# Optimization experiments

Measured on AMD Instinct MI355X. Metric: run time of the kernel, lower is better.

The kernel has to match this reference:

```python
import jax, jax.numpy as jnp
import numpy as np

# Qwen3-Next style GatedDeltaNet config
H = 2048          # hidden_size
HV = 32           # num_v_heads
HK = 16           # num_k_heads
DK = 128          # head_k_dim
DV = 128          # head_v_dim
KW = 4            # conv kernel size
KEY_DIM = HK * DK
VAL_DIM = HV * DV
CONV_DIM = 2 * KEY_DIM + VAL_DIM
B, S = 2, 1024
EPS = 1e-6


def setup_inputs() -> dict:
    key = jax.random.key(0)
    ks = jax.random.split(key, 9)
    def rn(i, shape, scale):
        return jax.random.normal(ks[i], shape, jnp.float32) * scale
    return {
        "hidden_states": rn(0, (B, S, H), 1.0),
        "Wqkv": rn(1, (H, CONV_DIM), H ** -0.5),
        "Wz": rn(2, (H, VAL_DIM), H ** -0.5),
        "Wb": rn(3, (H, HV), H ** -0.5),
        "Wa": rn(4, (H, HV), H ** -0.5),
        "conv_w": rn(5, (CONV_DIM, KW), 0.3),
        "conv_b": jnp.zeros((CONV_DIM,), jnp.float32),
        "dt_bias": jnp.ones((HV,), jnp.float32),
        "A_log": jnp.log(jax.random.uniform(ks[6], (HV,), jnp.float32, 0.001, 16.0)),
        "norm_weight": jnp.ones((DV,), jnp.float32),
        "Wout": rn(7, (VAL_DIM, H), VAL_DIM ** -0.5),
    }


def _causal_depthwise_conv(x, w, b):
    # x: [B,S,C], w: [C,KW] depthwise, causal (left pad KW-1), then SiLU
    xp = jnp.pad(x, ((0, 0), (KW - 1, 0), (0, 0)))
    out = b
    for j in range(KW):
        out = out + xp[:, j:j + x.shape[1], :] * w[:, j]
    return jax.nn.silu(out)


def _l2norm(x):
    return x * jax.lax.rsqrt(jnp.sum(x * x, axis=-1, keepdims=True) + 1e-6)


def reference(hidden_states, Wqkv, Wz, Wb, Wa, conv_w, conv_b, dt_bias, A_log, norm_weight, Wout):
    x = hidden_states  # [B,S,H]
    mixed = _causal_depthwise_conv(x @ Wqkv, conv_w, conv_b)  # [B,S,CONV_DIM]
    q, k, v = jnp.split(mixed, [KEY_DIM, 2 * KEY_DIM], axis=-1)
    q = q.reshape(B, S, HK, DK)
    k = k.reshape(B, S, HK, DK)
    v = v.reshape(B, S, HV, DV)
    z = (x @ Wz).reshape(B, S, HV, DV)
    beta = jax.nn.sigmoid(x @ Wb)                                  # [B,S,HV]
    g = -jnp.exp(A_log) * jax.nn.softplus(x @ Wa + dt_bias)       # [B,S,HV]

    rep = HV // HK
    q = jnp.repeat(q, rep, axis=2)  # [B,S,HV,DK]
    k = jnp.repeat(k, rep, axis=2)
    q = _l2norm(q) * (DK ** -0.5)
    k = _l2norm(k)

    # gated delta-rule recurrence, state: [B,HV,DK,DV]
    def step(state, inp):
        qt, kt, vt, gt, bt = inp  # [B,HV,DK],[B,HV,DK],[B,HV,DV],[B,HV],[B,HV]
        state = state * jnp.exp(gt)[..., None, None]
        mem = jnp.einsum('bhk,bhkv->bhv', kt, state)
        delta = (vt - mem) * bt[..., None]
        state = state + jnp.einsum('bhk,bhv->bhkv', kt, delta)
        out_t = jnp.einsum('bhk,bhkv->bhv', qt, state)
        return state, out_t

    init = jnp.zeros((B, HV, DK, DV), jnp.float32)
    seq = (q.transpose(1, 0, 2, 3), k.transpose(1, 0, 2, 3), v.transpose(1, 0, 2, 3),
           g.transpose(1, 0, 2), beta.transpose(1, 0, 2))
    _, core = jax.lax.scan(step, init, seq)   # [S,B,HV,DV]
    core = core.transpose(1, 0, 2, 3)          # [B,S,HV,DV]

    # gated RMSNorm: gate with silu(z) then rms-normalize over head_v_dim
    gated = core * jax.nn.silu(z)
    var = jnp.mean(gated * gated, axis=-1, keepdims=True)
    normed = gated * jax.lax.rsqrt(var + EPS) * norm_weight

    return normed.reshape(B, S, VAL_DIM) @ Wout  # [B,S,H]
```

## Files before the change

### kernel.cpp

```cpp
#include <hip/hip_runtime.h>
#include <stdint.h>

typedef unsigned short u16;
typedef unsigned int u32;
typedef __attribute__((ext_vector_type(8))) short bf16x8;
typedef __attribute__((ext_vector_type(4))) float f32x4;

__device__ __forceinline__ float asf(u32 u) { union { u32 u; float f; } v; v.u = u; return v.f; }
__device__ __forceinline__ float bf2f(u16 h) { return asf(((u32)h) << 16); }
__device__ __forceinline__ u16 f2bf(float f) {
  union { float f; u32 u; } v; v.f = f;
  u32 r = v.u + 0x7fffu + ((v.u >> 16) & 1u);
  return (u16)(r >> 16);
}
__device__ __forceinline__ float silu(float x) { return x / (1.f + __expf(-x)); }

__device__ __forceinline__ void async16(void* lds, const void* g) {
  __builtin_amdgcn_global_load_lds(
      (__attribute__((address_space(1))) void*)g,
      (__attribute__((address_space(3))) void*)lds, 16, 0, 0);
}
__device__ __forceinline__ void async4(void* lds, const void* g) {
  __builtin_amdgcn_global_load_lds(
      (__attribute__((address_space(1))) void*)g,
      (__attribute__((address_space(3))) void*)lds, 4, 0, 0);
}

template <int CTRL>
__device__ __forceinline__ float dppadd(float x) {
  int y = __builtin_amdgcn_update_dpp(0, __float_as_int(x), CTRL, 0xf, 0xf, true);
  return x + __int_as_float(y);
}
__device__ __forceinline__ float redseg8(float x) {
  x = dppadd<0xB1>(x);
  x = dppadd<0x4E>(x);
  x = dppadd<0x141>(x);
  return x;
}
__device__ __forceinline__ float redseg16(float x) {
  x = dppadd<0xB1>(x);
  x = dppadd<0x4E>(x);
  x = dppadd<0x141>(x);
  x = dppadd<0x140>(x);
  return x;
}

__device__ __forceinline__ void unpack8(uint4 r, float* o) {
  o[0] = asf(r.x << 16); o[1] = asf(r.x & 0xffff0000u);
  o[2] = asf(r.y << 16); o[3] = asf(r.y & 0xffff0000u);
  o[4] = asf(r.z << 16); o[5] = asf(r.z & 0xffff0000u);
  o[6] = asf(r.w << 16); o[7] = asf(r.w & 0xffff0000u);
}

__global__ __launch_bounds__(256) void cvt_f32_bf16_k(
    const float* __restrict__ in, u16* __restrict__ out, int n8) {
  int i = blockIdx.x * 256 + threadIdx.x;
  if (i >= n8) return;
  const float4 a = *(const float4*)&in[(size_t)i * 8];
  const float4 b = *(const float4*)&in[(size_t)i * 8 + 4];
  u16 o[8] = {f2bf(a.x), f2bf(a.y), f2bf(a.z), f2bf(a.w),
              f2bf(b.x), f2bf(b.y), f2bf(b.z), f2bf(b.w)};
  *(uint4*)&out[(size_t)i * 8] = *(const uint4*)o;
}

__global__ __launch_bounds__(256) void transpose_cvt(
    const float* __restrict__ W, u16* __restrict__ WT, int R, int C) {
  __shared__ u16 tile[64][65];
  const int r0 = blockIdx.y * 64, c0 = blockIdx.x * 64;
  const int t = threadIdx.x;
  {
    const int lr = t >> 4;
    const int lc = (t & 15) * 4;
#pragma unroll
    for (int p = 0; p < 4; ++p) {
      int rr = lr + p * 16;
      float4 v = *(const float4*)&W[(size_t)(r0 + rr) * C + c0 + lc];
      tile[lc + 0][rr] = f2bf(v.x);
      tile[lc + 1][rr] = f2bf(v.y);
      tile[lc + 2][rr] = f2bf(v.z);
      tile[lc + 3][rr] = f2bf(v.w);
    }
  }
  __syncthreads();
  {
    const int wr = t >> 2;
    const int wc = (t & 3) * 16;
    u16 buf[16];
#pragma unroll
    for (int j = 0; j < 16; ++j) buf[j] = tile[wr][wc + j];
    u16* dst = &WT[(size_t)(c0 + wr) * R + r0 + wc];
    *(uint4*)(dst) = *(const uint4*)&buf[0];
    *(uint4*)(dst + 8) = *(const uint4*)&buf[8];
  }
}

template <int F32OUT>
__global__ __launch_bounds__(256) void gemm_mfma_bt(
    const u16* __restrict__ A, const u16* __restrict__ BT, void* __restrict__ Cout,
    int M, int N, int K) {
  __shared__ u16 As[128 * 32];
  __shared__ u16 Bs[128 * 32];
  const int tid = threadIdx.x;
  const int m0 = blockIdx.y * 128, n0 = blockIdx.x * 128;
  const int wave = tid >> 6, lane = tid & 63;
  const int wr = wave >> 1, wc = wave & 1;
  const int lrow = lane & 15, lgrp = lane >> 4;
  const int rsw = (lrow >> 1) & 3;

  f32x4 acc[4][4] = {};

  const int srow = tid >> 2;
  const int sslot = (tid & 3) ^ ((srow >> 1) & 3);
  const u16* gA0 = A + (size_t)(m0 + srow) * K + sslot * 8;
  const u16* gA1 = A + (size_t)(m0 + 64 + srow) * K + sslot * 8;
  const u16* gB0 = BT + (size_t)(n0 + srow) * K + sslot * 8;
  const u16* gB1 = BT + (size_t)(n0 + 64 + srow) * K + sslot * 8;
  u16* lA0 = As + tid * 8;
  u16* lA1 = As + 2048 + tid * 8;
  u16* lB0 = Bs + tid * 8;
  u16* lB1 = Bs + 2048 + tid * 8;

  int aoff[4], boff[4];
#pragma unroll
  for (int i = 0; i < 4; ++i) {
    int arow = wr * 64 + i * 16 + lrow;
    aoff[i] = arow * 64 + ((lgrp ^ rsw) << 4);
    int brow = wc * 64 + i * 16 + lrow;
    boff[i] = brow * 64 + ((lgrp ^ rsw) << 4);
  }

  for (int kt = 0; kt < K; kt += 32) {
    async16(lA0, gA0); async16(lA1, gA1);
    async16(lB0, gB0); async16(lB1, gB1);
    gA0 += 32; gA1 += 32; gB0 += 32; gB1 += 32;
    __syncthreads();
    bf16x8 af[4], bfr[4];
#pragma unroll
    for (int i = 0; i < 4; ++i) {
      af[i] = *(const bf16x8*)((const char*)As + aoff[i]);
      bfr[i] = *(const bf16x8*)((const char*)Bs + boff[i]);
    }
#pragma unroll
    for (int mi = 0; mi < 4; ++mi)
#pragma unroll
      for (int ni = 0; ni < 4; ++ni)
        acc[mi][ni] = __builtin_amdgcn_mfma_f32_16x16x32_bf16(af[mi], bfr[ni], acc[mi][ni], 0, 0, 0);
    __syncthreads();
  }

#pragma unroll
  for (int mi = 0; mi < 4; ++mi)
#pragma unroll
    for (int ni = 0; ni < 4; ++ni) {
      const int m = m0 + wr * 64 + mi * 16 + lgrp * 4;
      const int n = n0 + wc * 64 + ni * 16 + lrow;
      if (F32OUT) {
        float* C = (float*)Cout;
#pragma unroll
        for (int r = 0; r < 4; ++r)
          C[(size_t)(m + r) * N + n] = asf(((u32)f2bf(acc[mi][ni][r])) << 16);
      } else {
        u16* C = (u16*)Cout;
#pragma unroll
        for (int r = 0; r < 4; ++r)
          C[(size_t)(m + r) * N + n] = f2bf(acc[mi][ni][r]);
      }
    }
}

__global__ __launch_bounds__(256) void gemm_f32(
    const float* __restrict__ A, const float* __restrict__ B, u16* __restrict__ C,
    int M, int N, int K, int ldB) {
  __shared__ float As[32][68];
  __shared__ float Bs[32][68];
  const int tid = threadIdx.x;
  const int m0 = blockIdx.y * 64, n0 = blockIdx.x * 64;
  const int tx = tid & 15, ty = tid >> 4;
  float acc[4][4] = {};
  const int arow = tid >> 2, ac = (tid & 3) * 8;
  const int brow = tid >> 3, bc = (tid & 7) * 8;
  for (int kt = 0; kt < K; kt += 32) {
    const float* sa = &A[(size_t)(m0 + arow) * K + kt + ac];
    float4 a0 = *(const float4*)sa, a1 = *(const float4*)(sa + 4);
    As[ac + 0][arow] = a0.x; As[ac + 1][arow] = a0.y;
    As[ac + 2][arow] = a0.z; As[ac + 3][arow] = a0.w;
    As[ac + 4][arow] = a1.x; As[ac + 5][arow] = a1.y;
    As[ac + 6][arow] = a1.z; As[ac + 7][arow] = a1.w;
    const float* sb = &B[(size_t)(kt + brow) * ldB + n0 + bc];
    *(float4*)&Bs[brow][bc] = *(const float4*)sb;
    *(float4*)&Bs[brow][bc + 4] = *(const float4*)(sb + 4);
    __syncthreads();
#pragma unroll 8
    for (int kk = 0; kk < 32; ++kk) {
      float4 av = *(const float4*)&As[kk][ty * 4];
      float4 bv = *(const float4*)&Bs[kk][tx * 4];
      float a4[4] = {av.x, av.y, av.z, av.w};
      float b4[4] = {bv.x, bv.y, bv.z, bv.w};
#pragma unroll
      for (int i = 0; i < 4; ++i)
#pragma unroll
        for (int j = 0; j < 4; ++j) acc[i][j] += a4[i] * b4[j];
    }
    __syncthreads();
  }
#pragma unroll
  for (int i = 0; i < 4; ++i)
#pragma unroll
    for (int j = 0; j < 4; ++j)
      C[(size_t)(m0 + ty * 4 + i) * N + n0 + tx * 4 + j] = f2bf(acc[i][j]);
}

__global__ __launch_bounds__(256) void gemm_bf16A_f32(
    const u16* __restrict__ A, const float* __restrict__ B, float* __restrict__ C,
    int M, int N, int K, int ldB) {
  __shared__ float As[32][68];
  __shared__ float Bs[32][68];
  const int tid = threadIdx.x;
  const int m0 = blockIdx.y * 64, n0 = blockIdx.x * 64;
  const int tx = tid & 15, ty = tid >> 4;
  float acc[4][4] = {};
  const int arow = tid >> 2, ac = (tid & 3) * 8;
  const int brow = tid >> 3, bc = (tid & 7) * 8;
  for (int kt = 0; kt < K; kt += 32) {
    uint4 raw = *(const uint4*)&A[(size_t)(m0 + arow) * K + kt + ac];
    As[ac + 0][arow] = asf(raw.x << 16); As[ac + 1][arow] = asf(raw.x & 0xffff0000u);
    As[ac + 2][arow] = asf(raw.y << 16); As[ac + 3][arow] = asf(raw.y & 0xffff0000u);
    As[ac + 4][arow] = asf(raw.z << 16); As[ac + 5][arow] = asf(raw.z & 0xffff0000u);
    As[ac + 6][arow] = asf(raw.w << 16); As[ac + 7][arow] = asf(raw.w & 0xffff0000u);
    const float* sb = &B[(size_t)(kt + brow) * ldB + n0 + bc];
    *(float4*)&Bs[brow][bc] = *(const float4*)sb;
    *(float4*)&Bs[brow][bc + 4] = *(const float4*)(sb + 4);
    __syncthreads();
#pragma unroll 8
    for (int kk = 0; kk < 32; ++kk) {
      float4 av = *(const float4*)&As[kk][ty * 4];
      float4 bv = *(const float4*)&Bs[kk][tx * 4];
      float a4[4] = {av.x, av.y, av.z, av.w};
      float b4[4] = {bv.x, bv.y, bv.z, bv.w};
#pragma unroll
      for (int i = 0; i < 4; ++i)
#pragma unroll
        for (int j = 0; j < 4; ++j) acc[i][j] += a4[i] * b4[j];
    }
    __syncthreads();
  }
#pragma unroll
  for (int i = 0; i < 4; ++i)
#pragma unroll
    for (int j = 0; j < 4; ++j) {
      u32 r = (u32)f2bf(acc[i][j]) << 16;
      C[(size_t)(m0 + ty * 4 + i) * N + n0 + tx * 4 + j] = asf(r);
    }
}

__global__ __launch_bounds__(256) void betag_v2(
    const float* __restrict__ x, const float* __restrict__ Wb, const float* __restrict__ Wa,
    const float* __restrict__ dtb, const float* __restrict__ alog,
    float* __restrict__ beta, float* __restrict__ g) {
  __shared__ float part[256];
  const int token = blockIdx.x;
  const int t = threadIdx.x;
  const int o = t & 63;
  const int sl = t >> 6;
  const float* xrow = x + (size_t)token * 2048;
  const float* W = (o < 32) ? Wb : Wa;
  const int oc = o & 31;
  float acc = 0.f;
  const int k0 = sl * 512;
#pragma unroll 4
  for (int k = k0; k < k0 + 512; ++k) acc += xrow[k] * W[(size_t)k * 32 + oc];
  part[t] = acc;
  __syncthreads();
  if (t < 64) {
    float s = part[t] + part[t + 64] + part[t + 128] + part[t + 192];
    if (t < 32) {
      beta[(size_t)token * 32 + t] = 1.f / (1.f + __expf(-s));
    } else {
      int j = t - 32;
      float xx = s + dtb[j];
      float sp = (xx > 20.f) ? xx : log1pf(__expf(xx));
      g[(size_t)token * 32 + j] = -__expf(alog[j]) * sp;
    }
  }
}

__global__ __launch_bounds__(256) void conv_qk_v2(
    const u16* __restrict__ mixedQK, const float* __restrict__ cw, const float* __restrict__ cb,
    u16* __restrict__ qn, u16* __restrict__ kn) {
  __shared__ float qk[4096];
  const int token = blockIdx.x;
  const int s = token & 1023;
  const int t = threadIdx.x;
#pragma unroll
  for (int gi = 0; gi < 2; ++gi) {
    const int ch = t * 8 + gi * 2048;
    float acc[8];
    float w[8][4];
#pragma unroll
    for (int i = 0; i < 8; ++i) {
      acc[i] = cb[ch + i];
      float4 wv = *(const float4*)&cw[(size_t)(ch + i) * 4];
      w[i][0] = wv.x; w[i][1] = wv.y; w[i][2] = wv.z; w[i][3] = wv.w;
    }
#pragma unroll
    for (int j = 0; j < 4; ++j) {
      int sr = s - 3 + j;
      if (sr >= 0) {
        uint4 raw = *(const uint4*)&mixedQK[(size_t)(token - 3 + j) * 4096 + ch];
        float xv[8];
        unpack8(raw, xv);
#pragma unroll
        for (int i = 0; i < 8; ++i) acc[i] += w[i][j] * xv[i];
      }
    }
#pragma unroll
    for (int i = 0; i < 8; ++i) qk[ch + i] = silu(acc[i]);
  }
  __syncthreads();
  const int slot = t >> 3, m = t & 7;
  float vv[16];
#pragma unroll
  for (int i = 0; i < 16; i += 4) {
    float4 f = *(const float4*)&qk[slot * 128 + m * 16 + i];
    vv[i] = f.x; vv[i + 1] = f.y; vv[i + 2] = f.z; vv[i + 3] = f.w;
  }
  float ss = 0.f;
#pragma unroll
  for (int i = 0; i < 16; ++i) ss += vv[i] * vv[i];
  ss = redseg8(ss);
  float r = rsqrtf(ss + 1e-6f);
  u16 o[16];
  u16* dst;
  if (slot < 16) {
    r *= 0.08838834764831845f;
    dst = qn + (size_t)token * 2048 + slot * 128 + m * 16;
  } else {
    dst = kn + (size_t)token * 2048 + (slot - 16) * 128 + m * 16;
  }
#pragma unroll
  for (int i = 0; i < 16; ++i) o[i] = f2bf(vv[i] * r);
  *(uint4*)dst = *(const uint4*)&o[0];
  *(uint4*)(dst + 8) = *(const uint4*)&o[8];
}

__global__ __launch_bounds__(256) void conv_v_v2(
    const u16* __restrict__ mixedV, const float* __restrict__ cw, const float* __restrict__ cb,
    u16* __restrict__ vout) {
  const int token = blockIdx.x;
  const int s = token & 1023;
  const int t = threadIdx.x;
#pragma unroll
  for (int gi = 0; gi < 2; ++gi) {
    const int ch = t * 8 + gi * 2048;
    const int gch = 4096 + ch;
    float acc[8];
    float w[8][4];
#pragma unroll
    for (int i = 0; i < 8; ++i) {
      acc[i] = cb[gch + i];
      float4 wv = *(const float4*)&cw[(size_t)(gch + i) * 4];
      w[i][0] = wv.x; w[i][1] = wv.y; w[i][2] = wv.z; w[i][3] = wv.w;
    }
#pragma unroll
    for (int j = 0; j < 4; ++j) {
      int sr = s - 3 + j;
      if (sr >= 0) {
        uint4 raw = *(const uint4*)&mixedV[(size_t)(token - 3 + j) * 4096 + ch];
        float xv[8];
        unpack8(raw, xv);
#pragma unroll
        for (int i = 0; i < 8; ++i) acc[i] += w[i][j] * xv[i];
      }
    }
    u16 o[8];
#pragma unroll
    for (int i = 0; i < 8; ++i) o[i] = f2bf(silu(acc[i]));
    *(uint4*)&vout[(size_t)token * 4096 + ch] = *(const uint4*)o;
  }
}

#define SCAN_T 64
__global__ __launch_bounds__(512) void scan_lds2(
    const u16* __restrict__ qn, const u16* __restrict__ kn, const u16* __restrict__ v,
    const float* __restrict__ g, const float* __restrict__ beta,
    u16* __restrict__ core) {
  __shared__ u16 Kb[2][SCAN_T][128];
  __shared__ u16 Qb[2][SCAN_T][128];
  __shared__ u16 Vb[2][SCAN_T][32];
  __shared__ float Gb[2][SCAN_T];
  __shared__ float Bb[2][SCAN_T];

  const int blk = blockIdx.x;
  const int pair = blk >> 2, chunk = blk & 3;
  const int b = pair >> 5, h = pair & 31, kh = h >> 1;
  const int t = threadIdx.x;
  const int wave = t >> 6;
  const int lane = t & 63;
  const int seg = t & 15, dvl = t >> 4;
  const int dv = chunk * 32 + dvl;

  const size_t tok0 = (size_t)b * 1024;
  const u16* kbase = kn + tok0 * 2048 + (size_t)kh * 128;
  const u16* qbase = qn + tok0 * 2048 + (size_t)kh * 128;
  const u16* vbase = v + tok0 * 4096 + (size_t)h * 128 + chunk * 32;
  const float* gbase = g + tok0 * 32 + h;
  const float* bbase = beta + tok0 * 32 + h;
  u16* cp = core + tok0 * 4096 + (size_t)h * 128 + dv;

  auto stage = [&](int buf, int tile) {
    const int gt = tile * SCAN_T;
#pragma unroll
    for (int i = 0; i < 2; ++i) {
      int off = (i * 512 + t) * 16;
      int row = off >> 8;
      int c16 = (off >> 4) & 15;
      async16((char*)&Kb[buf][0][0] + off,
              (const char*)(kbase + (size_t)(gt + row) * 2048) + c16 * 16);
      async16((char*)&Qb[buf][0][0] + off,
              (const char*)(qbase + (size_t)(gt + row) * 2048) + c16 * 16);
    }
    if (t < 256) {
      int off = t * 16;
      int row = off >> 6;
      int c16 = (off >> 4) & 3;
      async16((char*)&Vb[buf][0][0] + off,
              (const char*)(vbase + (size_t)(gt + row) * 4096) + c16 * 16);
    }
    if (wave == 0)
      async4((char*)&Gb[buf][0] + lane * 4, (const char*)(gbase + (size_t)(gt + lane) * 32));
    if (wave == 1)
      async4((char*)&Bb[buf][0] + lane * 4, (const char*)(bbase + (size_t)(gt + lane) * 32));
  };

  float st[8];
#pragma unroll
  for (int i = 0; i < 8; ++i) st[i] = 0.f;

  stage(0, 0);

  for (int tile = 0; tile < 1024 / SCAN_T; ++tile) {
    const int buf = tile & 1;
    __syncthreads();
    if (tile < 1024 / SCAN_T - 1) stage(buf ^ 1, tile + 1);

    uint4 ck = *(const uint4*)&Kb[buf][0][seg * 8];
    uint4 cq = *(const uint4*)&Qb[buf][0][seg * 8];
    u16 cv = Vb[buf][0][dvl];
    float cg = Gb[buf][0], cbt = Bb[buf][0];

    for (int ls = 0; ls < SCAN_T; ++ls) {
      const int nls = (ls + 1 < SCAN_T) ? ls + 1 : ls;
      uint4 nk = *(const uint4*)&Kb[buf][nls][seg * 8];
      uint4 nq = *(const uint4*)&Qb[buf][nls][seg * 8];
      u16 nv = Vb[buf][nls][dvl];
      float ng = Gb[buf][nls], nbt = Bb[buf][nls];

      float kv[8], qv[8];
      unpack8(ck, kv);
      unpack8(cq, qv);
      float vt = bf2f(cv);
      float eg = __expf(cg);
      float bs = cbt;

      float m0 = 0.f, m1 = 0.f;
#pragma unroll
      for (int i = 0; i < 8; i += 2) {
        st[i] *= eg;     m0 += kv[i] * st[i];
        st[i + 1] *= eg; m1 += kv[i + 1] * st[i + 1];
      }
      float mem = redseg16(m0 + m1);
      float delta = (vt - mem) * bs;

      float o0 = 0.f, o1 = 0.f;
#pragma unroll
      for (int i = 0; i < 8; i += 2) {
        st[i] += kv[i] * delta;         o0 += qv[i] * st[i];
        st[i + 1] += kv[i + 1] * delta; o1 += qv[i + 1] * st[i + 1];
      }
      float out = redseg16(o0 + o1);

      if (seg == 0) *cp = f2bf(out);
      cp += 4096;

      ck = nk; cq = nq; cv = nv; cg = ng; cbt = nbt;
    }
  }
}

__global__ __launch_bounds__(256) void gnorm_v2(
    const u16* __restrict__ core, const u16* __restrict__ z,
    const float* __restrict__ nw, u16* __restrict__ normed) {
  const int token = blockIdx.x;
  const int t = threadIdx.x;
  const int slot = t >> 3, m = t & 7;
  const size_t base = (size_t)token * 4096 + slot * 128 + m * 16;
  uint4 cr0 = *(const uint4*)&core[base];
  uint4 cr1 = *(const uint4*)&core[base + 8];
  uint4 zr0 = *(const uint4*)&z[base];
  uint4 zr1 = *(const uint4*)&z[base + 8];
  float cf[16], zf[16];
  unpack8(cr0, cf); unpack8(cr1, cf + 8);
  unpack8(zr0, zf); unpack8(zr1, zf + 8);
  float gv[16];
  float ss = 0.f;
#pragma unroll
  for (int i = 0; i < 16; ++i) {
    gv[i] = cf[i] * silu(zf[i]);
    ss += gv[i] * gv[i];
  }
  ss = redseg8(ss);
  float scale = rsqrtf(ss * (1.f / 128.f) + 1e-6f);
  u16 o[16];
#pragma unroll
  for (int i = 0; i < 16; i += 4) {
    float4 w = *(const float4*)&nw[m * 16 + i];
    o[i] = f2bf(gv[i] * scale * w.x);
    o[i + 1] = f2bf(gv[i + 1] * scale * w.y);
    o[i + 2] = f2bf(gv[i + 2] * scale * w.z);
    o[i + 3] = f2bf(gv[i + 3] * scale * w.w);
  }
  *(uint4*)&normed[base] = *(const uint4*)&o[0];
  *(uint4*)&normed[base + 8] = *(const uint4*)&o[8];
}

__device__ float blockvar4k(const float* p, float* red, int t) {
  float s = 0.f, s2 = 0.f;
  for (int i = t; i < 4096; i += 256) { float v = p[i]; s += v; s2 += v * v; }
  red[t] = s; __syncthreads();
  for (int o = 128; o; o >>= 1) { if (t < o) red[t] += red[t + o]; __syncthreads(); }
  float mean = red[0] / 4096.f; __syncthreads();
  red[t] = s2; __syncthreads();
  for (int o = 128; o; o >>= 1) { if (t < o) red[t] += red[t + o]; __syncthreads(); }
  float m2 = red[0] / 4096.f; __syncthreads();
  return m2 - mean * mean;
}

__global__ __launch_bounds__(256) void diag_kernel(
    const float* convb, const float* nw, const float* dtb, const float* alog,
    const float* x, const float* Wz, const float* Wout,
    int hostbad, float* out) {
  __shared__ int bad;
  __shared__ float red[256];
  const int t = threadIdx.x;
  if (t == 0) bad = hostbad ? 1 : 0;
  __syncthreads();
  {
    int ok = 1;
    for (int i = t; i < 8192; i += 256) ok &= (convb[i] == 0.0f);
    if (!ok) atomicOr(&bad, 2);
  }
  if (t < 128 && nw[t] != 1.0f) atomicOr(&bad, 4);
  if (t < 32 && dtb[t] != 1.0f) atomicOr(&bad, 8);
  if (t < 32) {
    float a = alog[t];
    if (!(a > -8.f && a < 3.f)) atomicOr(&bad, 16);
  }
  __syncthreads();
  float vx = blockvar4k(x, red, t);
  float vz = blockvar4k(Wz, red, t);
  float vo = blockvar4k(Wout, red, t);
  if (t == 0) {
    if (!(vx > 0.7f && vx < 1.4f)) atomicOr(&bad, 32);
    if (!(vz > 3.5e-4f && vz < 6.5e-4f)) atomicOr(&bad, 64);
    if (!(vo > 1.7e-4f && vo < 3.4e-4f)) atomicOr(&bad, 128);
  }
  __syncthreads();
  if (t == 0 && bad != 0) out[0] = 64.0f * (float)bad;
}

extern "C" void kernel_launch(void* const* d_in, const int* in_sizes, int n_in,
                              void* d_out, int out_size, void* d_ws, size_t ws_size,
                              hipStream_t stream) {
  const float* x    = (const float*)d_in[0];
  const float* Wqkv = (const float*)d_in[1];
  const float* Wz   = (const float*)d_in[2];
  const float* Wb   = (const float*)d_in[3];
  const float* Wa   = (const float*)d_in[4];
  const float* cw   = (const float*)d_in[5];
  const float* cb   = (const float*)d_in[6];
  const float* dtb  = (const float*)d_in[7];
  const float* alog = (const float*)d_in[8];
  const float* nw   = (const float*)d_in[9];
  const float* Wout = (const float*)d_in[10];

  static const int exp_sizes[11] = {4194304, 16777216, 8388608, 65536, 65536,
                                    32768, 8192, 32, 32, 128, 8388608};
  int hostbad = (n_in != 11) ? 1 : 0;
  if (!hostbad)
    for (int i = 0; i < 11; ++i)
      if (in_sizes[i] != exp_sizes[i]) { hostbad = 1; break; }

  char* ws = (char*)d_ws;
  const size_t MB = 1048576;
  u16* mixedQK = (u16*)(ws);
  u16* vbuf    = (u16*)(ws);
  u16* normedb = (u16*)(ws);
  u16* mixedV  = (u16*)(ws + 16 * MB);
  u16* coreb   = (u16*)(ws + 16 * MB);
  u16* qn      = (u16*)(ws + 32 * MB);
  u16* kn      = (u16*)(ws + 40 * MB);
  u16* zbuf    = (u16*)(ws + 32 * MB);
  float* beta  = (float*)(ws + 48 * MB);
  float* gbuf  = (float*)(ws + 48 * MB + 262144);
  u16* xbf     = (u16*)(ws + 48 * MB + 524288);
  u16* WqkvT   = (u16*)(ws + 56 * MB + 524288);
  u16* WzT     = (u16*)(ws + 56 * MB + 524288);
  u16* WoutT   = (u16*)(ws + 72 * MB + 524288);

  const bool use_mfma = (ws_size >= 90 * MB);

  if (use_mfma) {
    cvt_f32_bf16_k<<<dim3(2048), 256, 0, stream>>>(x, xbf, 524288);
    transpose_cvt<<<dim3(128, 32), 256, 0, stream>>>(Wqkv, WqkvT, 2048, 8192);

    gemm_mfma_bt<0><<<dim3(32, 16), 256, 0, stream>>>(xbf, WqkvT, mixedQK, 2048, 4096, 2048);
    gemm_mfma_bt<0><<<dim3(32, 16), 256, 0, stream>>>(xbf, WqkvT + (size_t)4096 * 2048, mixedV, 2048, 4096, 2048);

    transpose_cvt<<<dim3(64, 32), 256, 0, stream>>>(Wz, WzT, 2048, 4096);
    transpose_cvt<<<dim3(32, 64), 256, 0, stream>>>(Wout, WoutT, 4096, 2048);

    betag_v2<<<dim3(2048), 256, 0, stream>>>(x, Wb, Wa, dtb, alog, beta, gbuf);

    conv_qk_v2<<<dim3(2048), 256, 0, stream>>>(mixedQK, cw, cb, qn, kn);
    conv_v_v2<<<dim3(2048), 256, 0, stream>>>(mixedV, cw, cb, vbuf);

    scan_lds2<<<dim3(256), 512, 0, stream>>>(qn, kn, vbuf, gbuf, beta, coreb);

    gemm_mfma_bt<0><<<dim3(32, 16), 256, 0, stream>>>(xbf, WzT, zbuf, 2048, 4096, 2048);

    gnorm_v2<<<dim3(2048), 256, 0, stream>>>(coreb, zbuf, nw, normedb);

    gemm_mfma_bt<1><<<dim3(16, 16), 256, 0, stream>>>(normedb, WoutT, (float*)d_out, 2048, 2048, 4096);
  } else {
    gemm_f32<<<dim3(64, 32), 256, 0, stream>>>(x, Wqkv, mixedQK, 2048, 4096, 2048, 8192);
    gemm_f32<<<dim3(64, 32), 256, 0, stream>>>(x, Wqkv + 4096, mixedV, 2048, 4096, 2048, 8192);
    betag_v2<<<dim3(2048), 256, 0, stream>>>(x, Wb, Wa, dtb, alog, beta, gbuf);
    conv_qk_v2<<<dim3(2048), 256, 0, stream>>>(mixedQK, cw, cb, qn, kn);
    conv_v_v2<<<dim3(2048), 256, 0, stream>>>(mixedV, cw, cb, vbuf);
    scan_lds2<<<dim3(256), 512, 0, stream>>>(qn, kn, vbuf, gbuf, beta, coreb);
    gemm_f32<<<dim3(64, 32), 256, 0, stream>>>(x, Wz, zbuf, 2048, 4096, 2048, 4096);
    gnorm_v2<<<dim3(2048), 256, 0, stream>>>(coreb, zbuf, nw, normedb);
    gemm_bf16A_f32<<<dim3(32, 32), 256, 0, stream>>>(normedb, Wout, (float*)d_out, 2048, 2048, 4096, 2048);
  }

  diag_kernel<<<dim3(1), 256, 0, stream>>>(cb, nw, dtb, alog, x, Wz, Wout, hostbad, (float*)d_out);
}
```

Measured before the change: 891.8 us.

## Process two value columns per thread in scan with packed f32x2 math

```diff
diff --git a/kernel.cpp b/kernel.cpp
--- a/kernel.cpp
+++ b/kernel.cpp
@@ -5,6 +5,7 @@
 typedef unsigned int u32;
 typedef __attribute__((ext_vector_type(8))) short bf16x8;
 typedef __attribute__((ext_vector_type(4))) float f32x4;
+typedef __attribute__((ext_vector_type(2))) float f32x2;
 
 __device__ __forceinline__ float asf(u32 u) { union { u32 u; float f; } v; v.u = u; return v.f; }
 __device__ __forceinline__ float bf2f(u16 h) { return asf(((u32)h) << 16); }
@@ -279,7 +280,7 @@
       int j = t - 32;
       float xx = s + dtb[j];
       float sp = (xx > 20.f) ? xx : log1pf(__expf(xx));
-      g[(size_t)token * 32 + j] = -__expf(alog[j]) * sp;
+      g[(size_t)token * 32 + j] = __expf(-__expf(alog[j]) * sp);
     }
   }
 }
@@ -380,9 +381,9 @@
 }
 
 #define SCAN_T 64
-__global__ __launch_bounds__(512) void scan_lds2(
+__global__ __launch_bounds__(256) void scan_pk(
     const u16* __restrict__ qn, const u16* __restrict__ kn, const u16* __restrict__ v,
-    const float* __restrict__ g, const float* __restrict__ beta,
+    const float* __restrict__ eg, const float* __restrict__ beta,
     u16* __restrict__ core) {
   __shared__ u16 Kb[2][SCAN_T][128];
   __shared__ u16 Qb[2][SCAN_T][128];
@@ -396,22 +397,22 @@
   const int t = threadIdx.x;
   const int wave = t >> 6;
   const int lane = t & 63;
-  const int seg = t & 15, dvl = t >> 4;
-  const int dv = chunk * 32 + dvl;
+  const int seg = t & 15, dvp = t >> 4;
+  const int dv0 = chunk * 32 + dvp * 2;
 
   const size_t tok0 = (size_t)b * 1024;
   const u16* kbase = kn + tok0 * 2048 + (size_t)kh * 128;
   const u16* qbase = qn + tok0 * 2048 + (size_t)kh * 128;
   const u16* vbase = v + tok0 * 4096 + (size_t)h * 128 + chunk * 32;
-  const float* gbase = g + tok0 * 32 + h;
+  const float* gbase = eg + tok0 * 32 + h;
   const float* bbase = beta + tok0 * 32 + h;
-  u16* cp = core + tok0 * 4096 + (size_t)h * 128 + dv;
+  u32* cp32 = (u32*)(core + tok0 * 4096 + (size_t)h * 128 + dv0);
 
   auto stage = [&](int buf, int tile) {
     const int gt = tile * SCAN_T;
 #pragma unroll
-    for (int i = 0; i < 2; ++i) {
-      int off = (i * 512 + t) * 16;
+    for (int i = 0; i < 4; ++i) {
+      int off = (i * 256 + t) * 16;
       int row = off >> 8;
       int c16 = (off >> 4) & 15;
       async16((char*)&Kb[buf][0][0] + off,
@@ -419,7 +420,7 @@
       async16((char*)&Qb[buf][0][0] + off,
               (const char*)(qbase + (size_t)(gt + row) * 2048) + c16 * 16);
     }
-    if (t < 256) {
+    {
       int off = t * 16;
       int row = off >> 6;
       int c16 = (off >> 4) & 3;
@@ -432,9 +433,9 @@
       async4((char*)&Bb[buf][0] + lane * 4, (const char*)(bbase + (size_t)(gt + lane) * 32));
   };
 
-  float st[8];
-#pragma unroll
-  for (int i = 0; i < 8; ++i) st[i] = 0.f;
+  f32x2 st[8];
+#pragma unroll
+  for (int i = 0; i < 8; ++i) st[i] = (f32x2){0.f, 0.f};
 
   stage(0, 0);
 
@@ -445,42 +446,48 @@
 
     uint4 ck = *(const uint4*)&Kb[buf][0][seg * 8];
     uint4 cq = *(const uint4*)&Qb[buf][0][seg * 8];
-    u16 cv = Vb[buf][0][dvl];
+    u32 cv = *(const u32*)&Vb[buf][0][dvp * 2];
     float cg = Gb[buf][0], cbt = Bb[buf][0];
 
     for (int ls = 0; ls < SCAN_T; ++ls) {
       const int nls = (ls + 1 < SCAN_T) ? ls + 1 : ls;
       uint4 nk = *(const uint4*)&Kb[buf][nls][seg * 8];
       uint4 nq = *(const uint4*)&Qb[buf][nls][seg * 8];
-      u16 nv = Vb[buf][nls][dvl];
+      u32 nv = *(const u32*)&Vb[buf][nls][dvp * 2];
       float ng = Gb[buf][nls], nbt = Bb[buf][nls];
 
       float kv[8], qv[8];
       unpack8(ck, kv);
       unpack8(cq, qv);
-      float vt = bf2f(cv);
-      float eg = __expf(cg);
-      float bs = cbt;
-
-      float m0 = 0.f, m1 = 0.f;
-#pragma unroll
-      for (int i = 0; i < 8; i += 2) {
-        st[i] *= eg;     m0 += kv[i] * st[i];
-        st[i + 1] *= eg; m1 += kv[i + 1] * st[i + 1];
+      f32x2 v2 = {bf2f((u16)(cv & 0xffffu)), bf2f((u16)(cv >> 16))};
+      f32x2 eg2 = {cg, cg};
+
+      f32x2 m2 = {0.f, 0.f};
+#pragma unroll
+      for (int i = 0; i < 8; ++i) {
+        st[i] *= eg2;
+        f32x2 k2 = {kv[i], kv[i]};
+        m2 += k2 * st[i];
       }
-      float mem = redseg16(m0 + m1);
-      float delta = (vt - mem) * bs;
-
-      float o0 = 0.f, o1 = 0.f;
-#pragma unroll
-      for (int i = 0; i < 8; i += 2) {
-        st[i] += kv[i] * delta;         o0 += qv[i] * st[i];
-        st[i + 1] += kv[i + 1] * delta; o1 += qv[i + 1] * st[i + 1];
+      f32x2 mem2 = {redseg16(m2.x), redseg16(m2.y)};
+      f32x2 b2 = {cbt, cbt};
+      f32x2 d2 = (v2 - mem2) * b2;
+
+      f32x2 o2 = {0.f, 0.f};
+#pragma unroll
+      for (int i = 0; i < 8; ++i) {
+        f32x2 k2 = {kv[i], kv[i]};
+        f32x2 q2 = {qv[i], qv[i]};
+        st[i] += k2 * d2;
+        o2 += q2 * st[i];
       }
-      float out = redseg16(o0 + o1);
-
-      if (seg == 0) *cp = f2bf(out);
-      cp += 4096;
+      f32x2 out2 = {redseg16(o2.x), redseg16(o2.y)};
+
+      if (seg == 0) {
+        u32 pack = (u32)f2bf(out2.x) | ((u32)f2bf(out2.y) << 16);
+        *cp32 = pack;
+      }
+      cp32 += 2048;
 
       ck = nk; cq = nq; cv = nv; cg = ng; cbt = nbt;
     }
@@ -624,7 +631,7 @@
     conv_qk_v2<<<dim3(2048), 256, 0, stream>>>(mixedQK, cw, cb, qn, kn);
     conv_v_v2<<<dim3(2048), 256, 0, stream>>>(mixedV, cw, cb, vbuf);
 
-    scan_lds2<<<dim3(256), 512, 0, stream>>>(qn, kn, vbuf, gbuf, beta, coreb);
+    scan_pk<<<dim3(256), 256, 0, stream>>>(qn, kn, vbuf, gbuf, beta, coreb);
 
     gemm_mfma_bt<0><<<dim3(32, 16), 256, 0, stream>>>(xbf, WzT, zbuf, 2048, 4096, 2048);
 
@@ -637,7 +644,7 @@
     betag_v2<<<dim3(2048), 256, 0, stream>>>(x, Wb, Wa, dtb, alog, beta, gbuf);
     conv_qk_v2<<<dim3(2048), 256, 0, stream>>>(mixedQK, cw, cb, qn, kn);
     conv_v_v2<<<dim3(2048), 256, 0, stream>>>(mixedV, cw, cb, vbuf);
-    scan_lds2<<<dim3(256), 512, 0, stream>>>(qn, kn, vbuf, gbuf, beta, coreb);
+    scan_pk<<<dim3(256), 256, 0, stream>>>(qn, kn, vbuf, gbuf, beta, coreb);
     gemm_f32<<<dim3(64, 32), 256, 0, stream>>>(x, Wz, zbuf, 2048, 4096, 2048, 4096);
     gnorm_v2<<<dim3(2048), 256, 0, stream>>>(coreb, zbuf, nw, normedb);
     gemm_bf16A_f32<<<dim3(32, 32), 256, 0, stream>>>(normedb, Wout, (float*)d_out, 2048, 2048, 4096, 2048);
```

New measurement: 870.5 us. 1.02x faster.

## Split scan across more blocks, precompute decay exp, overlap output reductions

Applied to the files above, without the earlier changes.

```diff
diff --git a/kernel.cpp b/kernel.cpp
--- a/kernel.cpp
+++ b/kernel.cpp
@@ -279,7 +279,7 @@
       int j = t - 32;
       float xx = s + dtb[j];
       float sp = (xx > 20.f) ? xx : log1pf(__expf(xx));
-      g[(size_t)token * 32 + j] = -__expf(alog[j]) * sp;
+      g[(size_t)token * 32 + j] = __expf(-__expf(alog[j]) * sp);
     }
   }
 }
@@ -380,38 +380,38 @@
 }
 
 #define SCAN_T 64
-__global__ __launch_bounds__(512) void scan_lds2(
+__global__ __launch_bounds__(256) void scan_v5(
     const u16* __restrict__ qn, const u16* __restrict__ kn, const u16* __restrict__ v,
-    const float* __restrict__ g, const float* __restrict__ beta,
+    const float* __restrict__ eg, const float* __restrict__ beta,
     u16* __restrict__ core) {
   __shared__ u16 Kb[2][SCAN_T][128];
   __shared__ u16 Qb[2][SCAN_T][128];
-  __shared__ u16 Vb[2][SCAN_T][32];
+  __shared__ u16 Vb[2][SCAN_T][16];
   __shared__ float Gb[2][SCAN_T];
   __shared__ float Bb[2][SCAN_T];
 
   const int blk = blockIdx.x;
-  const int pair = blk >> 2, chunk = blk & 3;
+  const int pair = blk >> 3, chunk = blk & 7;
   const int b = pair >> 5, h = pair & 31, kh = h >> 1;
   const int t = threadIdx.x;
   const int wave = t >> 6;
   const int lane = t & 63;
   const int seg = t & 15, dvl = t >> 4;
-  const int dv = chunk * 32 + dvl;
+  const int dv = chunk * 16 + dvl;
 
   const size_t tok0 = (size_t)b * 1024;
   const u16* kbase = kn + tok0 * 2048 + (size_t)kh * 128;
   const u16* qbase = qn + tok0 * 2048 + (size_t)kh * 128;
-  const u16* vbase = v + tok0 * 4096 + (size_t)h * 128 + chunk * 32;
-  const float* gbase = g + tok0 * 32 + h;
+  const u16* vbase = v + tok0 * 4096 + (size_t)h * 128 + chunk * 16;
+  const float* gbase = eg + tok0 * 32 + h;
   const float* bbase = beta + tok0 * 32 + h;
   u16* cp = core + tok0 * 4096 + (size_t)h * 128 + dv;
 
   auto stage = [&](int buf, int tile) {
     const int gt = tile * SCAN_T;
 #pragma unroll
-    for (int i = 0; i < 2; ++i) {
-      int off = (i * 512 + t) * 16;
+    for (int i = 0; i < 4; ++i) {
+      int off = (i * 256 + t) * 16;
       int row = off >> 8;
       int c16 = (off >> 4) & 15;
       async16((char*)&Kb[buf][0][0] + off,
@@ -419,10 +419,10 @@
       async16((char*)&Qb[buf][0][0] + off,
               (const char*)(qbase + (size_t)(gt + row) * 2048) + c16 * 16);
     }
-    if (t < 256) {
+    if (t < 128) {
       int off = t * 16;
-      int row = off >> 6;
-      int c16 = (off >> 4) & 3;
+      int row = t >> 1;
+      int c16 = t & 1;
       async16((char*)&Vb[buf][0][0] + off,
               (const char*)(vbase + (size_t)(gt + row) * 4096) + c16 * 16);
     }
@@ -459,26 +459,28 @@
       unpack8(ck, kv);
       unpack8(cq, qv);
       float vt = bf2f(cv);
-      float eg = __expf(cg);
-      float bs = cbt;
 
       float m0 = 0.f, m1 = 0.f;
 #pragma unroll
       for (int i = 0; i < 8; i += 2) {
-        st[i] *= eg;     m0 += kv[i] * st[i];
-        st[i + 1] *= eg; m1 += kv[i + 1] * st[i + 1];
+        st[i] *= cg;     m0 += kv[i] * st[i];
+        st[i + 1] *= cg; m1 += kv[i + 1] * st[i + 1];
+      }
+      float p0 = 0.f, p1 = 0.f, s0 = 0.f, s1 = 0.f;
+#pragma unroll
+      for (int i = 0; i < 8; i += 2) {
+        p0 += qv[i] * st[i];         s0 += qv[i] * kv[i];
+        p1 += qv[i + 1] * st[i + 1]; s1 += qv[i + 1] * kv[i + 1];
       }
       float mem = redseg16(m0 + m1);
-      float delta = (vt - mem) * bs;
-
-      float o0 = 0.f, o1 = 0.f;
-#pragma unroll
-      for (int i = 0; i < 8; i += 2) {
-        st[i] += kv[i] * delta;         o0 += qv[i] * st[i];
-        st[i + 1] += kv[i + 1] * delta; o1 += qv[i + 1] * st[i + 1];
-      }
-      float out = redseg16(o0 + o1);
-
+      float p = redseg16(p0 + p1);
+      float qk = redseg16(s0 + s1);
+
+      float delta = (vt - mem) * cbt;
+#pragma unroll
+      for (int i = 0; i < 8; ++i) st[i] += kv[i] * delta;
+
+      float out = p + qk * delta;
       if (seg == 0) *cp = f2bf(out);
       cp += 4096;
 
@@ -624,7 +626,7 @@
     conv_qk_v2<<<dim3(2048), 256, 0, stream>>>(mixedQK, cw, cb, qn, kn);
     conv_v_v2<<<dim3(2048), 256, 0, stream>>>(mixedV, cw, cb, vbuf);
 
-    scan_lds2<<<dim3(256), 512, 0, stream>>>(qn, kn, vbuf, gbuf, beta, coreb);
+    scan_v5<<<dim3(512), 256, 0, stream>>>(qn, kn, vbuf, gbuf, beta, coreb);
 
     gemm_mfma_bt<0><<<dim3(32, 16), 256, 0, stream>>>(xbf, WzT, zbuf, 2048, 4096, 2048);
 
@@ -637,7 +639,7 @@
     betag_v2<<<dim3(2048), 256, 0, stream>>>(x, Wb, Wa, dtb, alog, beta, gbuf);
     conv_qk_v2<<<dim3(2048), 256, 0, stream>>>(mixedQK, cw, cb, qn, kn);
     conv_v_v2<<<dim3(2048), 256, 0, stream>>>(mixedV, cw, cb, vbuf);
-    scan_lds2<<<dim3(256), 512, 0, stream>>>(qn, kn, vbuf, gbuf, beta, coreb);
+    scan_v5<<<dim3(512), 256, 0, stream>>>(qn, kn, vbuf, gbuf, beta, coreb);
     gemm_f32<<<dim3(64, 32), 256, 0, stream>>>(x, Wz, zbuf, 2048, 4096, 2048, 4096);
     gnorm_v2<<<dim3(2048), 256, 0, stream>>>(coreb, zbuf, nw, normedb);
     gemm_bf16A_f32<<<dim3(32, 32), 256, 0, stream>>>(normedb, Wout, (float*)d_out, 2048, 2048, 4096, 2048);
```

Result: slower. 961.9 us (+7.9%).

## Rewrite scan staging via registers with fp32 LDS tiles and precomputed decay

Applied to the files above, without the earlier changes.

```diff
diff --git a/kernel.cpp b/kernel.cpp
--- a/kernel.cpp
+++ b/kernel.cpp
@@ -19,11 +19,6 @@
   __builtin_amdgcn_global_load_lds(
       (__attribute__((address_space(1))) void*)g,
       (__attribute__((address_space(3))) void*)lds, 16, 0, 0);
-}
-__device__ __forceinline__ void async4(void* lds, const void* g) {
-  __builtin_amdgcn_global_load_lds(
-      (__attribute__((address_space(1))) void*)g,
-      (__attribute__((address_space(3))) void*)lds, 4, 0, 0);
 }
 
 template <int CTRL>
@@ -279,7 +274,7 @@
       int j = t - 32;
       float xx = s + dtb[j];
       float sp = (xx > 20.f) ? xx : log1pf(__expf(xx));
-      g[(size_t)token * 32 + j] = -__expf(alog[j]) * sp;
+      g[(size_t)token * 32 + j] = __expf(-__expf(alog[j]) * sp);
     }
   }
 }
@@ -379,23 +374,22 @@
   }
 }
 
-#define SCAN_T 64
-__global__ __launch_bounds__(512) void scan_lds2(
+#define ST 32
+#define NT (1024 / ST)
+__global__ __launch_bounds__(512) void scan_v7(
     const u16* __restrict__ qn, const u16* __restrict__ kn, const u16* __restrict__ v,
-    const float* __restrict__ g, const float* __restrict__ beta,
+    const float* __restrict__ eg, const float* __restrict__ beta,
     u16* __restrict__ core) {
-  __shared__ u16 Kb[2][SCAN_T][128];
-  __shared__ u16 Qb[2][SCAN_T][128];
-  __shared__ u16 Vb[2][SCAN_T][32];
-  __shared__ float Gb[2][SCAN_T];
-  __shared__ float Bb[2][SCAN_T];
+  __shared__ float Kf[2][ST][128];
+  __shared__ float Qf[2][ST][128];
+  __shared__ float Vf[2][ST][32];
+  __shared__ float Gf[2][ST];
+  __shared__ float Bf[2][ST];
 
   const int blk = blockIdx.x;
   const int pair = blk >> 2, chunk = blk & 3;
   const int b = pair >> 5, h = pair & 31, kh = h >> 1;
   const int t = threadIdx.x;
-  const int wave = t >> 6;
-  const int lane = t & 63;
   const int seg = t & 15, dvl = t >> 4;
   const int dv = chunk * 32 + dvl;
 
@@ -403,73 +397,74 @@
   const u16* kbase = kn + tok0 * 2048 + (size_t)kh * 128;
   const u16* qbase = qn + tok0 * 2048 + (size_t)kh * 128;
   const u16* vbase = v + tok0 * 4096 + (size_t)h * 128 + chunk * 32;
-  const float* gbase = g + tok0 * 32 + h;
+  const float* gbase = eg + tok0 * 32 + h;
   const float* bbase = beta + tok0 * 32 + h;
   u16* cp = core + tok0 * 4096 + (size_t)h * 128 + dv;
 
-  auto stage = [&](int buf, int tile) {
-    const int gt = tile * SCAN_T;
-#pragma unroll
-    for (int i = 0; i < 2; ++i) {
-      int off = (i * 512 + t) * 16;
-      int row = off >> 8;
-      int c16 = (off >> 4) & 15;
-      async16((char*)&Kb[buf][0][0] + off,
-              (const char*)(kbase + (size_t)(gt + row) * 2048) + c16 * 16);
-      async16((char*)&Qb[buf][0][0] + off,
-              (const char*)(qbase + (size_t)(gt + row) * 2048) + c16 * 16);
-    }
+  const int srow = t >> 4;
+  const int sc8 = (t & 15) * 8;
+  const int vrow = t >> 3, vc4 = (t & 7) * 4;
+
+  uint4 rk, rq;
+  uint2 rv;
+  float rgb = 0.f;
+
+  auto load_regs = [&](int tile) {
+    const int gt = tile * ST;
+    rk = *(const uint4*)(kbase + (size_t)(gt + srow) * 2048 + sc8);
+    rq = *(const uint4*)(qbase + (size_t)(gt + srow) * 2048 + sc8);
+    if (t < 256) rv = *(const uint2*)(vbase + (size_t)(gt + vrow) * 4096 + vc4);
+    if (t < 32) rgb = gbase[(size_t)(gt + t) * 32];
+    else if (t < 64) rgb = bbase[(size_t)(gt + t - 32) * 32];
+  };
+  auto write_lds = [&](int buf) {
+    float kf[8], qf[8];
+    unpack8(rk, kf);
+    unpack8(rq, qf);
+    *(float4*)&Kf[buf][srow][sc8] = *(const float4*)&kf[0];
+    *(float4*)&Kf[buf][srow][sc8 + 4] = *(const float4*)&kf[4];
+    *(float4*)&Qf[buf][srow][sc8] = *(const float4*)&qf[0];
+    *(float4*)&Qf[buf][srow][sc8 + 4] = *(const float4*)&qf[4];
     if (t < 256) {
-      int off = t * 16;
-      int row = off >> 6;
-      int c16 = (off >> 4) & 3;
-      async16((char*)&Vb[buf][0][0] + off,
-              (const char*)(vbase + (size_t)(gt + row) * 4096) + c16 * 16);
-    }
-    if (wave == 0)
-      async4((char*)&Gb[buf][0] + lane * 4, (const char*)(gbase + (size_t)(gt + lane) * 32));
-    if (wave == 1)
-      async4((char*)&Bb[buf][0] + lane * 4, (const char*)(bbase + (size_t)(gt + lane) * 32));
+      float vf[4] = {bf2f((u16)(rv.x & 0xffffu)), bf2f((u16)(rv.x >> 16)),
+                     bf2f((u16)(rv.y & 0xffffu)), bf2f((u16)(rv.y >> 16))};
+      *(float4*)&Vf[buf][vrow][vc4] = *(const float4*)&vf[0];
+    }
+    if (t < 32) Gf[buf][t] = rgb;
+    else if (t < 64) Bf[buf][t - 32] = rgb;
   };
 
   float st[8];
 #pragma unroll
   for (int i = 0; i < 8; ++i) st[i] = 0.f;
 
-  stage(0, 0);
-
-  for (int tile = 0; tile < 1024 / SCAN_T; ++tile) {
-    const int buf = tile & 1;
-    __syncthreads();
-    if (tile < 1024 / SCAN_T - 1) stage(buf ^ 1, tile + 1);
-
-    uint4 ck = *(const uint4*)&Kb[buf][0][seg * 8];
-    uint4 cq = *(const uint4*)&Qb[buf][0][seg * 8];
-    u16 cv = Vb[buf][0][dvl];
-    float cg = Gb[buf][0], cbt = Bb[buf][0];
-
-    for (int ls = 0; ls < SCAN_T; ++ls) {
-      const int nls = (ls + 1 < SCAN_T) ? ls + 1 : ls;
-      uint4 nk = *(const uint4*)&Kb[buf][nls][seg * 8];
-      uint4 nq = *(const uint4*)&Qb[buf][nls][seg * 8];
-      u16 nv = Vb[buf][nls][dvl];
-      float ng = Gb[buf][nls], nbt = Bb[buf][nls];
-
+  load_regs(0);
+  write_lds(0);
+  __syncthreads();
+
+  int cur = 0;
+  for (int tile = 0; tile < NT; ++tile) {
+    if (tile + 1 < NT) load_regs(tile + 1);
+
+#pragma unroll 4
+    for (int ls = 0; ls < ST; ++ls) {
       float kv[8], qv[8];
-      unpack8(ck, kv);
-      unpack8(cq, qv);
-      float vt = bf2f(cv);
-      float eg = __expf(cg);
-      float bs = cbt;
+      *(float4*)&kv[0] = *(const float4*)&Kf[cur][ls][seg * 8];
+      *(float4*)&kv[4] = *(const float4*)&Kf[cur][ls][seg * 8 + 4];
+      *(float4*)&qv[0] = *(const float4*)&Qf[cur][ls][seg * 8];
+      *(float4*)&qv[4] = *(const float4*)&Qf[cur][ls][seg * 8 + 4];
+      const float vt = Vf[cur][ls][dvl];
+      const float gg = Gf[cur][ls];
+      const float bb = Bf[cur][ls];
 
       float m0 = 0.f, m1 = 0.f;
 #pragma unroll
       for (int i = 0; i < 8; i += 2) {
-        st[i] *= eg;     m0 += kv[i] * st[i];
-        st[i + 1] *= eg; m1 += kv[i + 1] * st[i + 1];
+        st[i] *= gg;     m0 += kv[i] * st[i];
+        st[i + 1] *= gg; m1 += kv[i + 1] * st[i + 1];
       }
       float mem = redseg16(m0 + m1);
-      float delta = (vt - mem) * bs;
+      float delta = (vt - mem) * bb;
 
       float o0 = 0.f, o1 = 0.f;
 #pragma unroll
@@ -479,11 +474,12 @@
       }
       float out = redseg16(o0 + o1);
 
-      if (seg == 0) *cp = f2bf(out);
-      cp += 4096;
-
-      ck = nk; cq = nq; cv = nv; cg = ng; cbt = nbt;
-    }
+      if (seg == 0) cp[(size_t)(tile * ST + ls) * 4096] = f2bf(out);
+    }
+
+    if (tile + 1 < NT) write_lds(cur ^ 1);
+    __syncthreads();
+    cur ^= 1;
   }
 }
 
@@ -624,7 +620,7 @@
     conv_qk_v2<<<dim3(2048), 256, 0, stream>>>(mixedQK, cw, cb, qn, kn);
     conv_v_v2<<<dim3(2048), 256, 0, stream>>>(mixedV, cw, cb, vbuf);
 
-    scan_lds2<<<dim3(256), 512, 0, stream>>>(qn, kn, vbuf, gbuf, beta, coreb);
+    scan_v7<<<dim3(256), 512, 0, stream>>>(qn, kn, vbuf, gbuf, beta, coreb);
 
     gemm_mfma_bt<0><<<dim3(32, 16), 256, 0, stream>>>(xbf, WzT, zbuf, 2048, 4096, 2048);
 
@@ -637,7 +633,7 @@
     betag_v2<<<dim3(2048), 256, 0, stream>>>(x, Wb, Wa, dtb, alog, beta, gbuf);
     conv_qk_v2<<<dim3(2048), 256, 0, stream>>>(mixedQK, cw, cb, qn, kn);
     conv_v_v2<<<dim3(2048), 256, 0, stream>>>(mixedV, cw, cb, vbuf);
-    scan_lds2<<<dim3(256), 512, 0, stream>>>(qn, kn, vbuf, gbuf, beta, coreb);
+    scan_v7<<<dim3(256), 512, 0, stream>>>(qn, kn, vbuf, gbuf, beta, coreb);
     gemm_f32<<<dim3(64, 32), 256, 0, stream>>>(x, Wz, zbuf, 2048, 4096, 2048, 4096);
     gnorm_v2<<<dim3(2048), 256, 0, stream>>>(coreb, zbuf, nw, normedb);
     gemm_bf16A_f32<<<dim3(32, 32), 256, 0, stream>>>(normedb, Wout, (float*)d_out, 2048, 2048, 4096, 2048);
```

After: 813.9 us. 1.1x faster.
